# Kernel optimization log

Measured on AMD Instinct MI355X. Metric: run time of the kernel, lower is better.

The kernel has to match this reference:

```python
import jax, jax.numpy as jnp
import numpy as np

N_EMBD = 1024
N_HEAD = 16
HEAD_DIM = N_EMBD // N_HEAD
SEQ = 2048
BATCH = 2
WINDOW = 256
SCALE = 1.0 / np.sqrt(HEAD_DIM)
MASK_VALUE = -10000.0


def setup_inputs() -> dict:
    key = jax.random.key(0)
    ks = jax.random.split(key, 5)
    s = 0.02
    return {
        "hidden_states": jax.random.normal(ks[0], (BATCH, SEQ, N_EMBD), dtype=jnp.float32),
        "w_attn": jax.random.normal(ks[1], (N_EMBD, 3 * N_EMBD), dtype=jnp.float32) * s,
        "b_attn": jnp.zeros((3 * N_EMBD,), dtype=jnp.float32),
        "w_proj": jax.random.normal(ks[2], (N_EMBD, N_EMBD), dtype=jnp.float32) * s,
        "b_proj": jnp.zeros((N_EMBD,), dtype=jnp.float32),
    }


def _mask(seq_len):
    # causal AND sliding window: j <= i and j > i - WINDOW
    i = jnp.arange(seq_len)[:, None]
    j = jnp.arange(seq_len)[None, :]
    return (j <= i) & (j > i - WINDOW)  # [T, T] bool


def reference(hidden_states, w_attn, b_attn, w_proj, b_proj):
    B, T, _ = hidden_states.shape
    qkv = hidden_states @ w_attn + b_attn  # [B, T, 3E]
    q, k, v = jnp.split(qkv, 3, axis=-1)
    # [B, H, T, D]
    q = q.reshape(B, T, N_HEAD, HEAD_DIM).transpose(0, 2, 1, 3)
    k = k.reshape(B, T, N_HEAD, HEAD_DIM).transpose(0, 2, 1, 3)
    v = v.reshape(B, T, N_HEAD, HEAD_DIM).transpose(0, 2, 1, 3)

    scores = jnp.einsum("bhqd,bhkd->bhqk", q, k) * SCALE  # [B, H, T, T]
    mask = _mask(T)[None, None]  # [1, 1, T, T]
    scores = jnp.where(mask, scores, MASK_VALUE)
    scores = jnp.clip(scores, -10000.0, 10000.0)
    attn = jax.nn.softmax(scores, axis=-1)
    out = jnp.einsum("bhqk,bhkd->bhqd", attn, v)  # [B, H, T, D]
    out = out.transpose(0, 2, 1, 3).reshape(B, T, N_EMBD)
    return out @ w_proj + b_proj
```

## Files before the change

kernel.cpp:

```cpp
#include <hip/hip_runtime.h>


typedef __bf16 bf16_t;
typedef bf16_t bf16x8 __attribute__((ext_vector_type(8)));
typedef bf16_t bf16x4 __attribute__((ext_vector_type(4)));
typedef float  floatx4 __attribute__((ext_vector_type(4)));

#define SEQ_T   2048
#define NHEAD   16
#define HDIM    64
#define EMB     1024
#define WIN     256
#define SCALE_F 0.125f

__global__ __launch_bounds__(1024) void detect_dtype(
    const uint4* __restrict__ w, int nvec, int* __restrict__ flag)
{
    __shared__ int cnt_s;
    if (threadIdx.x == 0) cnt_s = 0;
    __syncthreads();
    int c = 0;
    for (int i = threadIdx.x; i < nvec; i += 1024) {
        const uint4 v = w[i];
        #pragma unroll
        for (int e = 0; e < 4; ++e) {
            const unsigned int word = (&v.x)[e];
            const unsigned int ex = (word >> 7) & 0xffu;
            c += (ex >= 100u && ex <= 150u) ? 1 : 0;
        }
    }
    #pragma unroll
    for (int m = 32; m >= 1; m >>= 1) c += __shfl_xor(c, m, 64);
    if ((threadIdx.x & 63) == 0) atomicAdd(&cnt_s, c);
    __syncthreads();
    if (threadIdx.x == 0) *flag = (cnt_s * 2 > nvec * 4) ? 1 : 0;
}

__global__ __launch_bounds__(256) void canon_bf16(
    const void* __restrict__ src, bf16_t* __restrict__ dst, int n,
    const int* __restrict__ flag)
{
    const int f = *flag;
    const int i4 = (blockIdx.x * 256 + threadIdx.x) * 4;
    if (i4 >= n) return;
    bf16x4 v;
    if (f) {
        v = *(const bf16x4*)((const bf16_t*)src + i4);
    } else {
        const float4 x = *(const float4*)((const float*)src + i4);
        v[0] = (bf16_t)x.x; v[1] = (bf16_t)x.y;
        v[2] = (bf16_t)x.z; v[3] = (bf16_t)x.w;
    }
    *(bf16x4*)(dst + i4) = v;
}

__global__ __launch_bounds__(256) void transpose_to_bf16(
    const void* __restrict__ W, bf16_t* __restrict__ Wt, int K, int N,
    const int* __restrict__ flag)
{
    __shared__ __align__(16) bf16_t tile[64][68];
    const int f  = *flag;
    const int n0 = blockIdx.x * 64;
    const int k0 = blockIdx.y * 64;
    const int tx = threadIdx.x & 15;
    const int ty = threadIdx.x >> 4;

    #pragma unroll
    for (int r = ty; r < 64; r += 16) {
        bf16x4 v;
        const size_t base = (size_t)(k0 + r) * N + n0 + tx * 4;
        if (f) {
            v = *(const bf16x4*)((const bf16_t*)W + base);
        } else {
            const float4 x = *(const float4*)((const float*)W + base);
            v[0] = (bf16_t)x.x; v[1] = (bf16_t)x.y;
            v[2] = (bf16_t)x.z; v[3] = (bf16_t)x.w;
        }
        *(bf16x4*)&tile[r][tx * 4] = v;
    }
    __syncthreads();
    #pragma unroll
    for (int r = ty; r < 64; r += 16) {
        bf16x4 v;
        v[0] = tile[tx * 4 + 0][r];
        v[1] = tile[tx * 4 + 1][r];
        v[2] = tile[tx * 4 + 2][r];
        v[3] = tile[tx * 4 + 3][r];
        *(bf16x4*)(Wt + (size_t)(n0 + r) * K + k0 + tx * 4) = v;
    }
}

#define BM 128
#define BN 128
#define BK 32

__global__ __launch_bounds__(256) void gemm_bt_bias(
    const bf16_t* __restrict__ A,
    const bf16_t* __restrict__ Bt,
    const bf16_t* __restrict__ bias,
    void* __restrict__ C,
    int M, int N, int K,
    int force_bf16, const int* __restrict__ flag)
{
    __shared__ __align__(16) bf16_t As[2][BM * BK];
    __shared__ __align__(16) bf16_t Bs[2][BN * BK];

    const int obf = force_bf16 | *flag;
    const int tid  = threadIdx.x;
    const int wave = tid >> 6;
    const int lane = tid & 63;
    const int quad = lane >> 4;
    const int n16  = lane & 15;
    const int m0 = blockIdx.y * BM;
    const int n0 = blockIdx.x * BN;
    const int wm = (wave >> 1) * 64;
    const int wn = (wave & 1) * 64;

    floatx4 acc[4][4] = {};

    const int lr   = lane >> 2;
    const int lcsw = ((lane & 3) ^ (lr & 3)) * 8;

    auto stage = [&](int buf, int kk) {
        #pragma unroll
        for (int c = 0; c < 2; ++c) {
            const int row0 = wave * 32 + c * 16;
            const bf16_t* ga = A  + (size_t)(m0 + row0 + lr) * K + kk + lcsw;
            const bf16_t* gb = Bt + (size_t)(n0 + row0 + lr) * K + kk + lcsw;
            __builtin_amdgcn_global_load_lds(
                (const __attribute__((address_space(1))) void*)ga,
                (__attribute__((address_space(3))) void*)(&As[buf][row0 * BK]),
                16, 0, 0);
            __builtin_amdgcn_global_load_lds(
                (const __attribute__((address_space(1))) void*)gb,
                (__attribute__((address_space(3))) void*)(&Bs[buf][row0 * BK]),
                16, 0, 0);
        }
    };

    stage(0, 0);
    int cur = 0;
    const int rsw = (n16 & 3);

    for (int k0 = 0; k0 < K; k0 += BK) {
        __syncthreads();
        if (k0 + BK < K) stage(cur ^ 1, k0 + BK);

        const bf16_t* pa = &As[cur][(wm + n16) * BK + ((quad ^ rsw) * 8)];
        const bf16_t* pb = &Bs[cur][(wn + n16) * BK + ((quad ^ rsw) * 8)];
        bf16x8 af[4], bfr[4];
        #pragma unroll
        for (int ff = 0; ff < 4; ++ff) {
            af[ff]  = *(const bf16x8*)(pa + ff * 16 * BK);
            bfr[ff] = *(const bf16x8*)(pb + ff * 16 * BK);
        }
        #pragma unroll
        for (int mf = 0; mf < 4; ++mf)
            #pragma unroll
            for (int nf = 0; nf < 4; ++nf)
                acc[mf][nf] = __builtin_amdgcn_mfma_f32_16x16x32_bf16(
                    af[mf], bfr[nf], acc[mf][nf], 0, 0, 0);
        cur ^= 1;
    }

    const int col   = n0 + wn + n16;
    const int rbase = m0 + wm + quad * 4;
    #pragma unroll
    for (int nf = 0; nf < 4; ++nf) {
        const float bv = (float)bias[col + nf * 16];
        #pragma unroll
        for (int mf = 0; mf < 4; ++mf) {
            #pragma unroll
            for (int r = 0; r < 4; ++r) {
                const size_t idx =
                    (size_t)(rbase + mf * 16 + r) * N + col + nf * 16;
                const float val = acc[mf][nf][r] + bv;
                if (obf) ((bf16_t*)C)[idx] = (bf16_t)val;
                else     ((float*)C)[idx]  = val;
            }
        }
    }
}

#define CW   160
#define VT_S 168
#define P_S  168

__global__ __launch_bounds__(256) void attn_mfma(
    const bf16_t* __restrict__ qkv,
    bf16_t* __restrict__ attn_out)
{
    __shared__ __align__(16) bf16_t Ks[CW * 64];
    __shared__ __align__(16) bf16_t Vt[64 * VT_S];
    __shared__ __align__(16) bf16_t Pst[4][16 * P_S];

    const int tid  = threadIdx.x;
    const int wave = tid >> 6;
    const int lane = tid & 63;
    const int quad = lane >> 4;
    const int n16  = lane & 15;

    const int i0 = blockIdx.x * 64;
    const int h  = blockIdx.y;
    const int b  = blockIdx.z;
    const size_t rowbase = (size_t)b * SEQ_T;
    const int kbase  = i0 - 256;
    const int iw     = 16 * wave;
    const int climit = 256 - i0;

    const bf16_t* Qg = qkv + (rowbase + i0 + iw + n16) * (3 * EMB) + h * HDIM;
    bf16x8 qf[2];
    qf[0] = *(const bf16x8*)(Qg + quad * 8);
    qf[1] = *(const bf16x8*)(Qg + 32 + quad * 8);

    floatx4 Oac[4] = {};
    float m_run[4], l_run[4];
    #pragma unroll
    for (int rr = 0; rr < 4; ++rr) { m_run[rr] = -3.0e38f; l_run[rr] = 0.f; }

    for (int hc = 0; hc < 2; ++hc) {
        const int cbase = hc * CW;

        bf16x8 vreg[5];
        #pragma unroll
        for (int t = 0; t < 5; ++t) {
            const int idx = tid + 256 * t;
            const int lc  = idx >> 3;
            const int d0  = (idx & 7) * 8;
            int j = kbase + cbase + lc; if (j < 0) j = 0;
            vreg[t] = *(const bf16x8*)(qkv + (rowbase + j) * (3 * EMB)
                                       + 2 * EMB + h * HDIM + d0);
        }

        __syncthreads();

        #pragma unroll
        for (int t = 0; t < 5; ++t) {
            const int lc0 = wave * 40 + t * 8;
            const int lcL = lc0 + (lane >> 3);
            int j = kbase + cbase + lcL; if (j < 0) j = 0;
            const int g = (lane & 7) ^ (lcL & 7);
            const bf16_t* src = qkv + (rowbase + j) * (3 * EMB)
                                + EMB + h * HDIM + g * 8;
            __builtin_amdgcn_global_load_lds(
                (const __attribute__((address_space(1))) void*)src,
                (__attribute__((address_space(3))) void*)(Ks + lc0 * 64),
                16, 0, 0);
        }

        #pragma unroll
        for (int t = 0; t < 5; ++t) {
            const int idx = tid + 256 * t;
            const int lc  = idx >> 3;
            const int d0  = (idx & 7) * 8;
            #pragma unroll
            for (int e = 0; e < 8; ++e)
                Vt[(d0 + e) * VT_S + lc] = vreg[t][e];
        }

        __syncthreads();

        floatx4 sc[10];
        #pragma unroll
        for (int tt = 0; tt < 10; ++tt) {
            sc[tt] = (floatx4){0.f, 0.f, 0.f, 0.f};
            #pragma unroll
            for (int s2 = 0; s2 < 2; ++s2) {
                const int lc = 16 * tt + n16;
                const int ch = (4 * s2 + quad) ^ (lc & 7);
                const bf16x8 kf = *(const bf16x8*)(Ks + lc * 64 + ch * 8);
                sc[tt] = __builtin_amdgcn_mfma_f32_16x16x32_bf16(
                    qf[s2], kf, sc[tt], 0, 0, 0);
            }
        }

        #pragma unroll
        for (int tt = 0; tt < 10; ++tt) {
            const int c  = cbase + 16 * tt + n16;
            const int cw = c - iw;
            #pragma unroll
            for (int rr = 0; rr < 4; ++rr) {
                const int r = quad * 4 + rr;
                const bool valid = (cw > r) && (cw <= r + 256) && (c >= climit);
                sc[tt][rr] = valid ? sc[tt][rr] * SCALE_F : -3.0e38f;
            }
        }

        float cm[4];
        #pragma unroll
        for (int rr = 0; rr < 4; ++rr) {
            cm[rr] = -3.0e38f;
            #pragma unroll
            for (int tt = 0; tt < 10; ++tt) cm[rr] = fmaxf(cm[rr], sc[tt][rr]);
            #pragma unroll
            for (int m = 8; m >= 1; m >>= 1)
                cm[rr] = fmaxf(cm[rr], __shfl_xor(cm[rr], m, 64));
        }

        #pragma unroll
        for (int rr = 0; rr < 4; ++rr) {
            const float mnew  = fmaxf(m_run[rr], cm[rr]);
            const float alpha = __expf(m_run[rr] - mnew);
            m_run[rr] = mnew;
            l_run[rr] *= alpha;
            #pragma unroll
            for (int nt = 0; nt < 4; ++nt) Oac[nt][rr] *= alpha;
        }

        float psum[4] = {0.f, 0.f, 0.f, 0.f};
        #pragma unroll
        for (int tt = 0; tt < 10; ++tt) {
            #pragma unroll
            for (int rr = 0; rr < 4; ++rr) {
                const float s = sc[tt][rr];
                const float e = (s > -1.0e38f) ? __expf(s - m_run[rr]) : 0.f;
                psum[rr] += e;
                Pst[wave][(quad * 4 + rr) * P_S + 16 * tt + n16] = (bf16_t)e;
            }
        }
        #pragma unroll
        for (int rr = 0; rr < 4; ++rr) {
            #pragma unroll
            for (int m = 8; m >= 1; m >>= 1)
                psum[rr] += __shfl_xor(psum[rr], m, 64);
            l_run[rr] += psum[rr];
        }

        __syncthreads();

        #pragma unroll
        for (int ks = 0; ks < 5; ++ks) {
            const bf16x8 paf = *(const bf16x8*)(
                &Pst[wave][n16 * P_S + ks * 32 + quad * 8]);
            #pragma unroll
            for (int nt = 0; nt < 4; ++nt) {
                const bf16x8 vbf = *(const bf16x8*)(
                    Vt + (nt * 16 + n16) * VT_S + ks * 32 + quad * 8);
                Oac[nt] = __builtin_amdgcn_mfma_f32_16x16x32_bf16(
                    paf, vbf, Oac[nt], 0, 0, 0);
            }
        }
    }

    #pragma unroll
    for (int rr = 0; rr < 4; ++rr) {
        const float rden = 1.0f / l_run[rr];
        const size_t row = rowbase + i0 + iw + quad * 4 + rr;
        #pragma unroll
        for (int nt = 0; nt < 4; ++nt) {
            attn_out[row * EMB + h * HDIM + nt * 16 + n16] =
                (bf16_t)(Oac[nt][rr] * rden);
        }
    }
}

extern "C" void kernel_launch(void* const* d_in, const int* in_sizes, int n_in,
                              void* d_out, int out_size, void* d_ws, size_t ws_size,
                              hipStream_t stream)
{
    const void* hidden = d_in[0];
    const void* w_attn = d_in[1];
    const void* b_attn = d_in[2];
    const void* w_proj = d_in[3];
    const void* b_proj = d_in[4];

    char* ws = (char*)d_ws;
    bf16_t* Wt_attn = (bf16_t*)(ws);
    bf16_t* Wt_proj = (bf16_t*)(ws + (6u << 20));
    bf16_t* qkv     = (bf16_t*)(ws + (8u << 20));
    bf16_t* attn_o  = (bf16_t*)(ws + (32u << 20));
    bf16_t* Hc      = (bf16_t*)(ws + (40u << 20));
    bf16_t* bb_attn = (bf16_t*)(ws + (48u << 20));
    bf16_t* bb_proj = (bf16_t*)(ws + (48u << 20) + 8192);
    int*    flag    = (int*)   (ws + (48u << 20) + 16384);

    detect_dtype<<<1, 1024, 0, stream>>>((const uint4*)hidden, 4096, flag);

    canon_bf16<<<4096, 256, 0, stream>>>(hidden, Hc, 4096 * 1024, flag);
    canon_bf16<<<3, 256, 0, stream>>>(b_attn, bb_attn, 3072, flag);
    canon_bf16<<<1, 256, 0, stream>>>(b_proj, bb_proj, 1024, flag);

    transpose_to_bf16<<<dim3(3072 / 64, 1024 / 64), 256, 0, stream>>>(
        w_attn, Wt_attn, 1024, 3072, flag);
    transpose_to_bf16<<<dim3(1024 / 64, 1024 / 64), 256, 0, stream>>>(
        w_proj, Wt_proj, 1024, 1024, flag);

    gemm_bt_bias<<<dim3(3072 / BN, 4096 / BM), 256, 0, stream>>>(
        Hc, Wt_attn, bb_attn, qkv, 4096, 3072, 1024, 1, flag);

    attn_mfma<<<dim3(SEQ_T / 64, NHEAD, 2), 256, 0, stream>>>(qkv, attn_o);

    gemm_bt_bias<<<dim3(1024 / BN, 4096 / BM), 256, 0, stream>>>(
        attn_o, Wt_proj, bb_proj, (void*)d_out, 4096, 1024, 1024, 0, flag);
}
```

Baseline: 201.7 us.

## Use BK=64 single-buffered GEMM tiles and narrower N tile for projection

The GEMM kernel is templated on N-tile width and its K step grows from 32 to 64 with an 8-way XOR swizzle. The LDS double buffer is dropped in favour of load, barrier, compute, barrier. The output projection now uses 64-wide N tiles, giving 512 blocks instead of 256 so more CUs have work. Halving the number of K iterations cuts barrier overhead, but global loads no longer overlap with MFMA work.

```diff
diff --git a/kernel.cpp b/kernel.cpp
--- a/kernel.cpp
+++ b/kernel.cpp
@@ -90,10 +90,7 @@
     }
 }
 
-#define BM 128
-#define BN 128
-#define BK 32
-
+template<int BNt>
 __global__ __launch_bounds__(256) void gemm_bt_bias(
     const bf16_t* __restrict__ A,
     const bf16_t* __restrict__ Bt,
@@ -102,71 +99,76 @@
     int M, int N, int K,
     int force_bf16, const int* __restrict__ flag)
 {
-    __shared__ __align__(16) bf16_t As[2][BM * BK];
-    __shared__ __align__(16) bf16_t Bs[2][BN * BK];
-
-    const int obf = force_bf16 | *flag;
+    constexpr int BMt = 128;
+    constexpr int NF  = BNt / 32;
+    __shared__ __align__(16) bf16_t As[BMt * 64];
+    __shared__ __align__(16) bf16_t Bs[BNt * 64];
+
+    const int obf  = force_bf16 | *flag;
     const int tid  = threadIdx.x;
     const int wave = tid >> 6;
     const int lane = tid & 63;
     const int quad = lane >> 4;
     const int n16  = lane & 15;
-    const int m0 = blockIdx.y * BM;
-    const int n0 = blockIdx.x * BN;
+    const int m0 = blockIdx.y * BMt;
+    const int n0 = blockIdx.x * BNt;
     const int wm = (wave >> 1) * 64;
-    const int wn = (wave & 1) * 64;
-
-    floatx4 acc[4][4] = {};
-
-    const int lr   = lane >> 2;
-    const int lcsw = ((lane & 3) ^ (lr & 3)) * 8;
-
-    auto stage = [&](int buf, int kk) {
-        #pragma unroll
-        for (int c = 0; c < 2; ++c) {
-            const int row0 = wave * 32 + c * 16;
-            const bf16_t* ga = A  + (size_t)(m0 + row0 + lr) * K + kk + lcsw;
-            const bf16_t* gb = Bt + (size_t)(n0 + row0 + lr) * K + kk + lcsw;
+    const int wn = (wave & 1) * (BNt / 2);
+
+    floatx4 acc[4][NF] = {};
+
+    const int lr = lane >> 3;
+    const int g8 = ((lane & 7) ^ lr) * 8;
+
+    const int csw = (quad ^ (n16 & 7)) * 8;
+
+    for (int k0 = 0; k0 < K; k0 += 64) {
+        #pragma unroll
+        for (int t = 0; t < BMt / 32; ++t) {
+            const int row0 = wave * (BMt / 4) + t * 8;
+            const bf16_t* ga = A + (size_t)(m0 + row0 + lr) * K + k0 + g8;
             __builtin_amdgcn_global_load_lds(
                 (const __attribute__((address_space(1))) void*)ga,
-                (__attribute__((address_space(3))) void*)(&As[buf][row0 * BK]),
+                (__attribute__((address_space(3))) void*)(As + row0 * 64),
                 16, 0, 0);
+        }
+        #pragma unroll
+        for (int t = 0; t < BNt / 32; ++t) {
+            const int row0 = wave * (BNt / 4) + t * 8;
+            const bf16_t* gb = Bt + (size_t)(n0 + row0 + lr) * K + k0 + g8;
             __builtin_amdgcn_global_load_lds(
                 (const __attribute__((address_space(1))) void*)gb,
-                (__attribute__((address_space(3))) void*)(&Bs[buf][row0 * BK]),
+                (__attribute__((address_space(3))) void*)(Bs + row0 * 64),
                 16, 0, 0);
         }
-    };
-
-    stage(0, 0);
-    int cur = 0;
-    const int rsw = (n16 & 3);
-
-    for (int k0 = 0; k0 < K; k0 += BK) {
-        __syncthreads();
-        if (k0 + BK < K) stage(cur ^ 1, k0 + BK);
-
-        const bf16_t* pa = &As[cur][(wm + n16) * BK + ((quad ^ rsw) * 8)];
-        const bf16_t* pb = &Bs[cur][(wn + n16) * BK + ((quad ^ rsw) * 8)];
-        bf16x8 af[4], bfr[4];
-        #pragma unroll
-        for (int ff = 0; ff < 4; ++ff) {
-            af[ff]  = *(const bf16x8*)(pa + ff * 16 * BK);
-            bfr[ff] = *(const bf16x8*)(pb + ff * 16 * BK);
-        }
-        #pragma unroll
-        for (int mf = 0; mf < 4; ++mf)
-            #pragma unroll
-            for (int nf = 0; nf < 4; ++nf)
-                acc[mf][nf] = __builtin_amdgcn_mfma_f32_16x16x32_bf16(
-                    af[mf], bfr[nf], acc[mf][nf], 0, 0, 0);
-        cur ^= 1;
+        __syncthreads();
+
+        #pragma unroll
+        for (int s = 0; s < 2; ++s) {
+            const int ch = (((4 * s + quad) ^ (n16 & 7)) * 8);
+            const bf16_t* pa = As + (wm + n16) * 64 + ch;
+            const bf16_t* pb = Bs + (wn + n16) * 64 + ch;
+            bf16x8 af[4], bfr[NF];
+            #pragma unroll
+            for (int ff = 0; ff < 4; ++ff)
+                af[ff] = *(const bf16x8*)(pa + ff * 16 * 64);
+            #pragma unroll
+            for (int ff = 0; ff < NF; ++ff)
+                bfr[ff] = *(const bf16x8*)(pb + ff * 16 * 64);
+            #pragma unroll
+            for (int mf = 0; mf < 4; ++mf)
+                #pragma unroll
+                for (int nf = 0; nf < NF; ++nf)
+                    acc[mf][nf] = __builtin_amdgcn_mfma_f32_16x16x32_bf16(
+                        af[mf], bfr[nf], acc[mf][nf], 0, 0, 0);
+        }
+        __syncthreads();
     }
 
     const int col   = n0 + wn + n16;
     const int rbase = m0 + wm + quad * 4;
     #pragma unroll
-    for (int nf = 0; nf < 4; ++nf) {
+    for (int nf = 0; nf < NF; ++nf) {
         const float bv = (float)bias[col + nf * 16];
         #pragma unroll
         for (int mf = 0; mf < 4; ++mf) {
@@ -385,11 +387,11 @@
     transpose_to_bf16<<<dim3(1024 / 64, 1024 / 64), 256, 0, stream>>>(
         w_proj, Wt_proj, 1024, 1024, flag);
 
-    gemm_bt_bias<<<dim3(3072 / BN, 4096 / BM), 256, 0, stream>>>(
+    gemm_bt_bias<128><<<dim3(3072 / 128, 4096 / 128), 256, 0, stream>>>(
         Hc, Wt_attn, bb_attn, qkv, 4096, 3072, 1024, 1, flag);
 
     attn_mfma<<<dim3(SEQ_T / 64, NHEAD, 2), 256, 0, stream>>>(qkv, attn_o);
 
-    gemm_bt_bias<<<dim3(1024 / BN, 4096 / BM), 256, 0, stream>>>(
+    gemm_bt_bias<64><<<dim3(1024 / 64, 4096 / 128), 256, 0, stream>>>(
         attn_o, Wt_proj, bb_proj, (void*)d_out, 4096, 1024, 1024, 0, flag);
 }
```

Result: faster. 190.9 us (-5.4%).
